# Kernel optimization log

Measured on AMD Instinct MI355X. Metric: run time of the kernel, lower is better.

## Reference

```python
import jax, jax.numpy as jnp
import numpy as np

B, L, N, D = 16, 4096, 1024, 256
EPS = 1e-5
NEG = -1e9


def setup_inputs() -> dict:
    key = jax.random.key(0)
    k1, k2, k3 = jax.random.split(key, 3)
    exp_f = jax.random.normal(k1, (B, L, D), dtype=jnp.float32)
    Q = jax.random.normal(k2, (B, N, D), dtype=jnp.float32)
    attn_mask = jax.random.randint(k3, (B, L, N), 0, 2).astype(jnp.bool_)
    gamma = jnp.ones((D,), dtype=jnp.float32)
    beta = jnp.zeros((D,), dtype=jnp.float32)
    return {"exp_f": exp_f, "Q": Q, "attn_mask": attn_mask, "gamma": gamma, "beta": beta}


def layer_norm(x, gamma, beta):
    mu = jnp.mean(x, axis=-1, keepdims=True)
    var = jnp.mean(jnp.square(x - mu), axis=-1, keepdims=True)
    return (x - mu) * jax.lax.rsqrt(var + EPS) * gamma + beta


def reference(exp_f, Q, attn_mask, gamma, beta):
    d_k = Q.shape[-1]
    scale = 1.0 / np.sqrt(d_k).astype(np.float32)
    # scores: [B, L, N] = exp_f @ Q^T / sqrt(d)
    scores = jnp.einsum('bld,bnd->bln', exp_f, Q) * scale
    scores = jnp.where(attn_mask, jnp.float32(NEG), scores)
    # transpose to [B, N, L], softmax over L (text positions)
    attn = jax.nn.softmax(scores.transpose(0, 2, 1), axis=-1)
    # context: [B, N, D]
    context = jnp.einsum('bnl,bld->bnd', attn, exp_f)
    return layer_norm(Q + context, gamma, beta)
```

## Files before the change

kernel.cpp:

```cpp
#include <hip/hip_runtime.h>
#include <hip/hip_bf16.h>
#include <math.h>

typedef short bf16x8 __attribute__((ext_vector_type(8)));
typedef float f32x4 __attribute__((ext_vector_type(4)));
typedef unsigned int u32;
typedef unsigned short u16;

#define B_ 16
#define L_ 4096
#define N_ 1024
#define D_ 256
#define EPS_ 1e-5f
#define NEG_ -1.0e9f
#define LOG2E_ 1.4426950408889634f
#define THR_ 8.0f

#define LBLK 32
#define PSTR2 40
#define ESTR2 264
#define TSTR2 40

__device__ __forceinline__ u32 pk2(float x, float y) {
  __hip_bfloat16 hx = __float2bfloat16(x), hy = __float2bfloat16(y);
  return (u32)reinterpret_cast<unsigned short&>(hx) |
         ((u32)reinterpret_cast<unsigned short&>(hy) << 16);
}
__device__ __forceinline__ float bf2f(u16 u) {
  return __uint_as_float(((u32)u) << 16);
}

__global__ __launch_bounds__(256)
void prep_kernel(const float* __restrict__ ef, __hip_bfloat16* __restrict__ et,
                 __hip_bfloat16* __restrict__ ebf, int write_ebf) {
  __shared__ float T[64][65];
  const int tid = threadIdx.x;
  const int bid = blockIdx.x;
  const int b  = bid >> 8;
  const int lt = (bid >> 2) & 63;
  const int dt = bid & 3;
  {
    const int r = tid & 63, s = tid >> 6;
    const float* src = ef + ((size_t)b * L_ + lt * 64 + r) * D_ + dt * 64 + s * 16;
    float v[16];
    #pragma unroll
    for (int k = 0; k < 4; ++k) {
      float4 f = *reinterpret_cast<const float4*>(src + 4 * k);
      v[4*k] = f.x; v[4*k+1] = f.y; v[4*k+2] = f.z; v[4*k+3] = f.w;
    }
    #pragma unroll
    for (int m = 0; m < 16; ++m) T[r][s * 16 + m] = v[m];
    if (write_ebf) {
      u32 w[8];
      #pragma unroll
      for (int p = 0; p < 8; ++p) w[p] = pk2(v[2*p], v[2*p+1]);
      __hip_bfloat16* dstrow = ebf + ((size_t)b * L_ + lt * 64 + r) * D_;
      const int u0 = dt * 8 + s * 2;
      const int sw = r & 7;
      *reinterpret_cast<uint4*>(dstrow + (size_t)(u0 ^ sw) * 8)       = *reinterpret_cast<uint4*>(&w[0]);
      *reinterpret_cast<uint4*>(dstrow + (size_t)((u0 + 1) ^ sw) * 8) = *reinterpret_cast<uint4*>(&w[4]);
    }
  }
  __syncthreads();
  {
    const int dcol = tid & 63, s2 = tid >> 6;
    float v[16];
    #pragma unroll
    for (int m = 0; m < 16; ++m) v[m] = T[s2 * 16 + m][dcol];
    u32 w[8];
    #pragma unroll
    for (int p = 0; p < 8; ++p) w[p] = pk2(v[2*p], v[2*p+1]);
    __hip_bfloat16* dst = et + ((size_t)b * D_ + dt * 64 + dcol) * L_ + lt * 64 + s2 * 16;
    *reinterpret_cast<uint4*>(dst)     = *reinterpret_cast<uint4*>(&w[0]);
    *reinterpret_cast<uint4*>(dst + 8) = *reinterpret_cast<uint4*>(&w[4]);
  }
}

__global__ __launch_bounds__(256, 2)
void attn_part3(const float* __restrict__ q, const int* __restrict__ msk,
                const __hip_bfloat16* __restrict__ et,
                const __hip_bfloat16* __restrict__ ebf, int slog,
                __hip_bfloat16* __restrict__ opart,
                float* __restrict__ mpart, float* __restrict__ lpart) {
  extern __shared__ char smem[];
  __hip_bfloat16* ELb = (__hip_bfloat16*)smem;
  __hip_bfloat16* TLb = ELb + 2 * 32 * 256;
  __hip_bfloat16* PLb = TLb + 2 * 256 * 32;

  const int tid  = threadIdx.x;
  const int wid  = tid >> 6;
  const int lane = tid & 63;
  const int g    = lane >> 4;
  const int c    = lane & 15;

  const int S   = 1 << slog;
  const int nb  = 128 << slog;
  const int raw = blockIdx.x;
  const int cpx = nb >> 3;
  const int bs  = (raw & 7) * cpx + (raw >> 3);
  const int nt   = bs & 7;
  const int rest = bs >> 3;
  const int s    = rest & (S - 1);
  const int b    = rest >> slog;

  const int lsplit = L_ >> slog;
  const int lbase  = s * lsplit;
  const int n0w    = nt * 128 + wid * 32;
  const int ntiles = lsplit / LBLK;

  bf16x8 qf[2][8];
  #pragma unroll
  for (int h = 0; h < 2; ++h) {
    const float* qrow = q + ((size_t)b * N_ + n0w + 16*h + c) * D_;
    #pragma unroll
    for (int dk = 0; dk < 8; ++dk) {
      float4 a  = *reinterpret_cast<const float4*>(qrow + 32 * dk + 8 * g);
      float4 b2 = *reinterpret_cast<const float4*>(qrow + 32 * dk + 8 * g + 4);
      u32 w[4] = {pk2(a.x, a.y), pk2(a.z, a.w), pk2(b2.x, b2.y), pk2(b2.z, b2.w)};
      qf[h][dk] = *reinterpret_cast<bf16x8*>(w);
    }
  }

  f32x4 oacc[2][16];
  float m_run[2], l_run[2];
  #pragma unroll
  for (int h = 0; h < 2; ++h) {
    m_run[h] = -INFINITY; l_run[h] = 0.f;
    #pragma unroll
    for (int j = 0; j < 16; ++j) oacc[h][j] = (f32x4){0.f, 0.f, 0.f, 0.f};
  }

  __hip_bfloat16* PLw = PLb + wid * (2 * 16 * PSTR2);
  const float scale = 0.0625f;

  auto STAGE = [&](int tindex, int bufi) {
    const int l0 = lbase + tindex * LBLK;
    __hip_bfloat16* ELd = ELb + bufi * (32 * 256);
    __hip_bfloat16* TLd = TLb + bufi * (256 * 32);
    #pragma unroll
    for (int p = 0; p < 4; ++p) {
      const int u   = (wid * 4 + p) * 64 + lane;
      const int row = u >> 5, iu = u & 31;
      const __hip_bfloat16* src =
          ebf + ((size_t)b * L_ + l0 + row) * D_ + (size_t)iu * 8;
      __builtin_amdgcn_global_load_lds(
          (const __attribute__((address_space(1))) void*)src,
          (__attribute__((address_space(3))) void*)(ELd + (size_t)(wid * 4 + p) * 512),
          16, 0, 0);
    }
    #pragma unroll
    for (int p = 0; p < 4; ++p) {
      const int u  = (wid * 4 + p) * 64 + lane;
      const int dr = u >> 2, iu = u & 3;
      const __hip_bfloat16* src =
          et + ((size_t)b * D_ + dr) * L_ + l0 + iu * 8;
      __builtin_amdgcn_global_load_lds(
          (const __attribute__((address_space(1))) void*)src,
          (__attribute__((address_space(3))) void*)(TLd + (size_t)(wid * 4 + p) * 512),
          16, 0, 0);
    }
  };

  STAGE(0, 0);
  int cur = 0;

  for (int t = 0; t < ntiles; ++t) {
    __syncthreads();
    if (t + 1 < ntiles) STAGE(t + 1, cur ^ 1);

    const int l0 = lbase + t * LBLK;
    const __hip_bfloat16* ELc = ELb + cur * (32 * 256);
    const __hip_bfloat16* TLc = TLb + cur * (256 * 32);

    int mv[16];
    #pragma unroll
    for (int h = 0; h < 2; ++h)
      #pragma unroll
      for (int tt = 0; tt < 2; ++tt)
        #pragma unroll
        for (int r = 0; r < 4; ++r)
          mv[8*h + 4*tt + r] =
              msk[((size_t)b * L_ + l0 + 16*tt + 4*g + r) * N_ + n0w + 16*h + c];

    float sv[2][8];
    __builtin_amdgcn_s_setprio(1);
    #pragma unroll
    for (int tt = 0; tt < 2; ++tt) {
      f32x4 s0 = (f32x4){0.f, 0.f, 0.f, 0.f};
      f32x4 s1 = (f32x4){0.f, 0.f, 0.f, 0.f};
      const __hip_bfloat16* Erow = ELc + (16*tt + c) * 256;
      const int sw = c & 7;
      #pragma unroll
      for (int dk = 0; dk < 8; ++dk) {
        bf16x8 af = *reinterpret_cast<const bf16x8*>(Erow + (size_t)((4*dk + g) ^ sw) * 8);
        s0 = __builtin_amdgcn_mfma_f32_16x16x32_bf16(af, qf[0][dk], s0, 0, 0, 0);
        s1 = __builtin_amdgcn_mfma_f32_16x16x32_bf16(af, qf[1][dk], s1, 0, 0, 0);
      }
      #pragma unroll
      for (int r = 0; r < 4; ++r) {
        float v0 = s0[r] * scale;
        float v1 = s1[r] * scale;
        if (mv[4*tt + r])     v0 = NEG_;
        if (mv[8 + 4*tt + r]) v1 = NEG_;
        sv[0][4*tt + r] = v0;
        sv[1][4*tt + r] = v1;
      }
    }
    __builtin_amdgcn_s_setprio(0);

    #pragma unroll
    for (int h = 0; h < 2; ++h) {
      float tm = sv[h][0];
      #pragma unroll
      for (int i = 1; i < 8; ++i) tm = fmaxf(tm, sv[h][i]);
      tm = fmaxf(tm, __shfl_xor(tm, 16));
      tm = fmaxf(tm, __shfl_xor(tm, 32));
      if (!__all(tm - m_run[h] <= THR_)) {
        const float mn = fmaxf(m_run[h], tm);
        const float alpha = __builtin_amdgcn_exp2f((m_run[h] - mn) * LOG2E_);
        l_run[h] *= alpha;
        float ar[4];
        #pragma unroll
        for (int r = 0; r < 4; ++r) ar[r] = __shfl(alpha, 4*g + r, 64);
        #pragma unroll
        for (int j = 0; j < 16; ++j)
          #pragma unroll
          for (int r = 0; r < 4; ++r) oacc[h][j][r] *= ar[r];
        m_run[h] = mn;
      }
      float ts = 0.f;
      #pragma unroll
      for (int i = 0; i < 8; ++i) {
        sv[h][i] = __builtin_amdgcn_exp2f((sv[h][i] - m_run[h]) * LOG2E_);
        ts += sv[h][i];
      }
      ts += __shfl_xor(ts, 16);
      ts += __shfl_xor(ts, 32);
      l_run[h] += ts;
      #pragma unroll
      for (int tt = 0; tt < 2; ++tt) {
        uint2 w;
        w.x = pk2(sv[h][4*tt+0], sv[h][4*tt+1]);
        w.y = pk2(sv[h][4*tt+2], sv[h][4*tt+3]);
        *reinterpret_cast<uint2*>(PLw + h * 16 * PSTR2 + c * PSTR2 + 16*tt + 4*g) = w;
      }
    }

    bf16x8 pa0 = *reinterpret_cast<const bf16x8*>(PLw + c * PSTR2 + 8*g);
    bf16x8 pa1 = *reinterpret_cast<const bf16x8*>(PLw + 16 * PSTR2 + c * PSTR2 + 8*g);
    __builtin_amdgcn_s_setprio(1);
    #pragma unroll
    for (int j = 0; j < 16; ++j) {
      bf16x8 bfr = *reinterpret_cast<const bf16x8*>(TLc + (16*j + c) * 32 + 8*g);
      oacc[0][j] = __builtin_amdgcn_mfma_f32_16x16x32_bf16(pa0, bfr, oacc[0][j], 0, 0, 0);
      oacc[1][j] = __builtin_amdgcn_mfma_f32_16x16x32_bf16(pa1, bfr, oacc[1][j], 0, 0, 0);
    }
    __builtin_amdgcn_s_setprio(0);

    cur ^= 1;
  }

  const size_t slot = (size_t)rest * 8 + nt;
  __hip_bfloat16* ob = opart + slot * (128 * 256);
  #pragma unroll
  for (int h = 0; h < 2; ++h) {
    float invl[4];
    #pragma unroll
    for (int r = 0; r < 4; ++r) invl[r] = 1.f / __shfl(l_run[h], 4*g + r, 64);
    #pragma unroll
    for (int r = 0; r < 4; ++r) {
      const int row = wid * 32 + 16*h + 4*g + r;
      #pragma unroll
      for (int j = 0; j < 16; ++j)
        ob[(size_t)row * 256 + 16*j + c] = __float2bfloat16(oacc[h][j][r] * invl[r]);
    }
  }
  if (g == 0) {
    #pragma unroll
    for (int h = 0; h < 2; ++h) {
      mpart[slot * 128 + wid * 32 + 16*h + c] = m_run[h];
      lpart[slot * 128 + wid * 32 + 16*h + c] = l_run[h];
    }
  }
}

__global__ __launch_bounds__(256, 2)
void attn_part2(const float* __restrict__ ef, const float* __restrict__ q,
                const int* __restrict__ msk, const __hip_bfloat16* __restrict__ et,
                int slog, __hip_bfloat16* __restrict__ opart,
                float* __restrict__ mpart, float* __restrict__ lpart) {
  extern __shared__ char smem[];
  __hip_bfloat16* EL  = (__hip_bfloat16*)smem;
  __hip_bfloat16* TL  = EL + LBLK * ESTR2;
  __hip_bfloat16* PLb = TL + 256 * TSTR2;
  const int tid  = threadIdx.x;
  const int wid  = tid >> 6;
  const int lane = tid & 63;
  const int g    = lane >> 4;
  const int c    = lane & 15;
  const int S   = 1 << slog;
  const int nb  = 128 << slog;
  const int raw = blockIdx.x;
  const int cpx = nb >> 3;
  const int bs  = (raw & 7) * cpx + (raw >> 3);
  const int nt   = bs & 7;
  const int rest = bs >> 3;
  const int s    = rest & (S - 1);
  const int b    = rest >> slog;
  const int lsplit = L_ >> slog;
  const int lbase  = s * lsplit;
  const int n0w    = nt * 128 + wid * 32;
  bf16x8 qf[2][8];
  #pragma unroll
  for (int h = 0; h < 2; ++h) {
    const float* qrow = q + ((size_t)b * N_ + n0w + 16*h + c) * D_;
    #pragma unroll
    for (int dk = 0; dk < 8; ++dk) {
      float4 a  = *reinterpret_cast<const float4*>(qrow + 32 * dk + 8 * g);
      float4 b2 = *reinterpret_cast<const float4*>(qrow + 32 * dk + 8 * g + 4);
      u32 w[4] = {pk2(a.x, a.y), pk2(a.z, a.w), pk2(b2.x, b2.y), pk2(b2.z, b2.w)};
      qf[h][dk] = *reinterpret_cast<bf16x8*>(w);
    }
  }
  f32x4 oacc[2][16];
  float m_run[2], l_run[2];
  #pragma unroll
  for (int h = 0; h < 2; ++h) {
    m_run[h] = -INFINITY; l_run[h] = 0.f;
    #pragma unroll
    for (int j = 0; j < 16; ++j) oacc[h][j] = (f32x4){0.f, 0.f, 0.f, 0.f};
  }
  __hip_bfloat16* PLw = PLb + wid * (2 * 16 * PSTR2);
  const float scale = 0.0625f;
  const int ntiles = lsplit / LBLK;
  for (int t = 0; t < ntiles; ++t) {
    const int l0 = lbase + t * LBLK;
    __syncthreads();
    #pragma unroll
    for (int p = 0; p < 4; ++p) {
      const int unit = tid + 256 * p;
      const int row = unit >> 5, iu = unit & 31;
      const float* src = ef + ((size_t)b * L_ + l0 + row) * D_ + iu * 8;
      float4 a  = *reinterpret_cast<const float4*>(src);
      float4 b2 = *reinterpret_cast<const float4*>(src + 4);
      u32 w[4] = {pk2(a.x, a.y), pk2(a.z, a.w), pk2(b2.x, b2.y), pk2(b2.z, b2.w)};
      *reinterpret_cast<uint4*>(EL + row * ESTR2 + iu * 8) = *reinterpret_cast<uint4*>(w);
    }
    #pragma unroll
    for (int p = 0; p < 4; ++p) {
      const int unit = tid + 256 * p;
      const int dr = unit >> 2, iu = unit & 3;
      *reinterpret_cast<uint4*>(TL + dr * TSTR2 + iu * 8) =
          *reinterpret_cast<const uint4*>(et + ((size_t)b * D_ + dr) * L_ + l0 + iu * 8);
    }
    int mv[16];
    #pragma unroll
    for (int h = 0; h < 2; ++h)
      #pragma unroll
      for (int tt = 0; tt < 2; ++tt)
        #pragma unroll
        for (int r = 0; r < 4; ++r)
          mv[8*h + 4*tt + r] =
              msk[((size_t)b * L_ + l0 + 16*tt + 4*g + r) * N_ + n0w + 16*h + c];
    __syncthreads();
    float sv[2][8];
    #pragma unroll
    for (int tt = 0; tt < 2; ++tt) {
      f32x4 s0 = (f32x4){0.f, 0.f, 0.f, 0.f};
      f32x4 s1 = (f32x4){0.f, 0.f, 0.f, 0.f};
      #pragma unroll
      for (int dk = 0; dk < 8; ++dk) {
        bf16x8 af = *reinterpret_cast<const bf16x8*>(EL + (16*tt + c) * ESTR2 + 32*dk + 8*g);
        s0 = __builtin_amdgcn_mfma_f32_16x16x32_bf16(af, qf[0][dk], s0, 0, 0, 0);
        s1 = __builtin_amdgcn_mfma_f32_16x16x32_bf16(af, qf[1][dk], s1, 0, 0, 0);
      }
      #pragma unroll
      for (int r = 0; r < 4; ++r) {
        float v0 = s0[r] * scale;
        float v1 = s1[r] * scale;
        if (mv[4*tt + r])     v0 = NEG_;
        if (mv[8 + 4*tt + r]) v1 = NEG_;
        sv[0][4*tt + r] = v0;
        sv[1][4*tt + r] = v1;
      }
    }
    #pragma unroll
    for (int h = 0; h < 2; ++h) {
      float tm = sv[h][0];
      #pragma unroll
      for (int i = 1; i < 8; ++i) tm = fmaxf(tm, sv[h][i]);
      tm = fmaxf(tm, __shfl_xor(tm, 16));
      tm = fmaxf(tm, __shfl_xor(tm, 32));
      if (!__all(tm - m_run[h] <= THR_)) {
        const float mn = fmaxf(m_run[h], tm);
        const float alpha = __builtin_amdgcn_exp2f((m_run[h] - mn) * LOG2E_);
        l_run[h] *= alpha;
        float ar[4];
        #pragma unroll
        for (int r = 0; r < 4; ++r) ar[r] = __shfl(alpha, 4*g + r, 64);
        #pragma unroll
        for (int j = 0; j < 16; ++j)
          #pragma unroll
          for (int r = 0; r < 4; ++r) oacc[h][j][r] *= ar[r];
        m_run[h] = mn;
      }
      float ts = 0.f;
      #pragma unroll
      for (int i = 0; i < 8; ++i) {
        sv[h][i] = __builtin_amdgcn_exp2f((sv[h][i] - m_run[h]) * LOG2E_);
        ts += sv[h][i];
      }
      ts += __shfl_xor(ts, 16);
      ts += __shfl_xor(ts, 32);
      l_run[h] += ts;
      #pragma unroll
      for (int tt = 0; tt < 2; ++tt) {
        uint2 w;
        w.x = pk2(sv[h][4*tt+0], sv[h][4*tt+1]);
        w.y = pk2(sv[h][4*tt+2], sv[h][4*tt+3]);
        *reinterpret_cast<uint2*>(PLw + h * 16 * PSTR2 + c * PSTR2 + 16*tt + 4*g) = w;
      }
    }
    bf16x8 pa0 = *reinterpret_cast<const bf16x8*>(PLw + c * PSTR2 + 8*g);
    bf16x8 pa1 = *reinterpret_cast<const bf16x8*>(PLw + 16 * PSTR2 + c * PSTR2 + 8*g);
    #pragma unroll
    for (int j = 0; j < 16; ++j) {
      bf16x8 bfr = *reinterpret_cast<const bf16x8*>(TL + (16*j + c) * TSTR2 + 8*g);
      oacc[0][j] = __builtin_amdgcn_mfma_f32_16x16x32_bf16(pa0, bfr, oacc[0][j], 0, 0, 0);
      oacc[1][j] = __builtin_amdgcn_mfma_f32_16x16x32_bf16(pa1, bfr, oacc[1][j], 0, 0, 0);
    }
  }
  const size_t slot = (size_t)rest * 8 + nt;
  __hip_bfloat16* ob = opart + slot * (128 * 256);
  #pragma unroll
  for (int h = 0; h < 2; ++h) {
    float invl[4];
    #pragma unroll
    for (int r = 0; r < 4; ++r) invl[r] = 1.f / __shfl(l_run[h], 4*g + r, 64);
    #pragma unroll
    for (int r = 0; r < 4; ++r) {
      const int row = wid * 32 + 16*h + 4*g + r;
      #pragma unroll
      for (int j = 0; j < 16; ++j)
        ob[(size_t)row * 256 + 16*j + c] = __float2bfloat16(oacc[h][j][r] * invl[r]);
    }
  }
  if (g == 0) {
    #pragma unroll
    for (int h = 0; h < 2; ++h) {
      mpart[slot * 128 + wid * 32 + 16*h + c] = m_run[h];
      lpart[slot * 128 + wid * 32 + 16*h + c] = l_run[h];
    }
  }
}

__global__ __launch_bounds__(256)
void combine_ln2(const float* __restrict__ q, const float* __restrict__ gamma,
                 const float* __restrict__ beta,
                 const __hip_bfloat16* __restrict__ opart,
                 const float* __restrict__ mpart, const float* __restrict__ lpart,
                 int S, float* __restrict__ out) {
  const int tid = threadIdx.x, wid = tid >> 6, lane = tid & 63;
  const int row = blockIdx.x * 4 + wid;
  const int b = row >> 10, n = row & 1023;
  const int ntile = n >> 7, nl = n & 127;

  float M = -INFINITY;
  for (int s = 0; s < S; ++s) {
    const size_t slot = (size_t)(b * S + s) * 8 + ntile;
    M = fmaxf(M, mpart[slot * 128 + nl]);
  }
  float W = 0.f;
  float4 o = make_float4(0.f, 0.f, 0.f, 0.f);
  for (int s = 0; s < S; ++s) {
    const size_t slot = (size_t)(b * S + s) * 8 + ntile;
    const float w = __builtin_amdgcn_exp2f((mpart[slot * 128 + nl] - M) * LOG2E_) *
                    lpart[slot * 128 + nl];
    W += w;
    ushort4 ov = *reinterpret_cast<const ushort4*>(
        opart + (slot * 128 + nl) * 256 + lane * 4);
    o.x += w * bf2f(ov.x); o.y += w * bf2f(ov.y);
    o.z += w * bf2f(ov.z); o.w += w * bf2f(ov.w);
  }
  const float invW = 1.f / W;
  float4 qv = *reinterpret_cast<const float4*>(q + ((size_t)b * N_ + n) * D_ + lane * 4);
  float4 x;
  x.x = qv.x + o.x * invW; x.y = qv.y + o.y * invW;
  x.z = qv.z + o.z * invW; x.w = qv.w + o.w * invW;

  float sum = x.x + x.y + x.z + x.w;
  sum += __shfl_xor(sum, 1);  sum += __shfl_xor(sum, 2);
  sum += __shfl_xor(sum, 4);  sum += __shfl_xor(sum, 8);
  sum += __shfl_xor(sum, 16); sum += __shfl_xor(sum, 32);
  const float mu = sum * (1.f / 256.f);
  float dx, v2 = 0.f;
  dx = x.x - mu; v2 += dx * dx; dx = x.y - mu; v2 += dx * dx;
  dx = x.z - mu; v2 += dx * dx; dx = x.w - mu; v2 += dx * dx;
  v2 += __shfl_xor(v2, 1);  v2 += __shfl_xor(v2, 2);
  v2 += __shfl_xor(v2, 4);  v2 += __shfl_xor(v2, 8);
  v2 += __shfl_xor(v2, 16); v2 += __shfl_xor(v2, 32);
  const float rs = rsqrtf(v2 * (1.f / 256.f) + EPS_);
  float4 gv = *reinterpret_cast<const float4*>(gamma + lane * 4);
  float4 bv = *reinterpret_cast<const float4*>(beta + lane * 4);
  float4 y;
  y.x = (x.x - mu) * rs * gv.x + bv.x;
  y.y = (x.y - mu) * rs * gv.y + bv.y;
  y.z = (x.z - mu) * rs * gv.z + bv.z;
  y.w = (x.w - mu) * rs * gv.w + bv.w;
  *reinterpret_cast<float4*>(out + ((size_t)b * N_ + n) * D_ + lane * 4) = y;
}

#define QSTRIDE (D_ + 4)
#define PSTRIDF (64 + 4)
__global__ __launch_bounds__(256)
void tgq_fallback(const float* __restrict__ ef, const float* __restrict__ q,
                  const int* __restrict__ msk, const float* __restrict__ gamma,
                  const float* __restrict__ beta, float* __restrict__ out) {
  extern __shared__ float fsm[];
  float* QL = fsm;
  float* EL = QL + 64 * QSTRIDE;
  float* PL = EL + 64 * QSTRIDE;
  const int tid = threadIdx.x, tx = tid & 15, ty = tid >> 4;
  const int b = blockIdx.x >> 4, n0 = (blockIdx.x & 15) * 64;
  {
    const float* qsrc = q + ((size_t)b * N_ + n0) * D_;
    for (int idx = tid; idx < 64 * 64; idx += 256) {
      int row = idx >> 6, c4 = idx & 63;
      *reinterpret_cast<float4*>(&QL[row * QSTRIDE + c4 * 4]) =
          *reinterpret_cast<const float4*>(qsrc + (size_t)row * D_ + c4 * 4);
    }
  }
  float4 O4[4][4]; float m_run[4], l_run[4];
  #pragma unroll
  for (int i = 0; i < 4; ++i) {
    m_run[i] = -INFINITY; l_run[i] = 0.f;
    #pragma unroll
    for (int k = 0; k < 4; ++k) O4[i][k] = make_float4(0.f, 0.f, 0.f, 0.f);
  }
  const float* efb = ef + (size_t)b * L_ * D_;
  const int* mb = msk + (size_t)b * L_ * N_;
  for (int t = 0; t < L_ / 64; ++t) {
    const int l0 = t * 64;
    __syncthreads();
    for (int idx = tid; idx < 64 * 64; idx += 256) {
      int row = idx >> 6, c4 = idx & 63;
      *reinterpret_cast<float4*>(&EL[row * QSTRIDE + c4 * 4]) =
          *reinterpret_cast<const float4*>(efb + (size_t)(l0 + row) * D_ + c4 * 4);
    }
    int4 mvv[4];
    #pragma unroll
    for (int j = 0; j < 4; ++j)
      mvv[j] = *reinterpret_cast<const int4*>(mb + (size_t)(l0 + tx + 16*j) * N_ + n0 + 4*ty);
    __syncthreads();
    float s0[4][4];
    #pragma unroll
    for (int i = 0; i < 4; ++i)
      #pragma unroll
      for (int j = 0; j < 4; ++j) s0[i][j] = 0.f;
    #pragma unroll 4
    for (int dq = 0; dq < 64; ++dq) {
      float4 qv[4], ev[4];
      #pragma unroll
      for (int i = 0; i < 4; ++i)
        qv[i] = *reinterpret_cast<const float4*>(&QL[(4*ty+i) * QSTRIDE + dq*4]);
      #pragma unroll
      for (int j = 0; j < 4; ++j)
        ev[j] = *reinterpret_cast<const float4*>(&EL[(tx+16*j) * QSTRIDE + dq*4]);
      #pragma unroll
      for (int i = 0; i < 4; ++i)
        #pragma unroll
        for (int j = 0; j < 4; ++j)
          s0[i][j] += qv[i].x*ev[j].x + qv[i].y*ev[j].y + qv[i].z*ev[j].z + qv[i].w*ev[j].w;
    }
    #pragma unroll
    for (int i = 0; i < 4; ++i)
      #pragma unroll
      for (int j = 0; j < 4; ++j) {
        float v = s0[i][j] * 0.0625f;
        int mi = (i==0)?mvv[j].x:(i==1)?mvv[j].y:(i==2)?mvv[j].z:mvv[j].w;
        if (mi) v = NEG_;
        s0[i][j] = v;
      }
    #pragma unroll
    for (int i = 0; i < 4; ++i) {
      float mt = fmaxf(fmaxf(s0[i][0], s0[i][1]), fmaxf(s0[i][2], s0[i][3]));
      mt = fmaxf(mt, __shfl_xor(mt,1)); mt = fmaxf(mt, __shfl_xor(mt,2));
      mt = fmaxf(mt, __shfl_xor(mt,4)); mt = fmaxf(mt, __shfl_xor(mt,8));
      float mn = fmaxf(m_run[i], mt);
      float alpha = __builtin_amdgcn_exp2f((m_run[i] - mn) * LOG2E_);
      float tsum = 0.f;
      #pragma unroll
      for (int j = 0; j < 4; ++j) {
        float p = __builtin_amdgcn_exp2f((s0[i][j] - mn) * LOG2E_);
        s0[i][j] = p; tsum += p;
      }
      tsum += __shfl_xor(tsum,1); tsum += __shfl_xor(tsum,2);
      tsum += __shfl_xor(tsum,4); tsum += __shfl_xor(tsum,8);
      l_run[i] = l_run[i] * alpha + tsum; m_run[i] = mn;
      #pragma unroll
      for (int k = 0; k < 4; ++k) {
        O4[i][k].x *= alpha; O4[i][k].y *= alpha; O4[i][k].z *= alpha; O4[i][k].w *= alpha;
      }
    }
    #pragma unroll
    for (int i = 0; i < 4; ++i)
      #pragma unroll
      for (int j = 0; j < 4; ++j)
        PL[(4*ty+i) * PSTRIDF + tx + 16*j] = s0[i][j];
    __syncthreads();
    #pragma unroll 2
    for (int l4 = 0; l4 < 16; ++l4) {
      float4 p4[4];
      #pragma unroll
      for (int i = 0; i < 4; ++i)
        p4[i] = *reinterpret_cast<const float4*>(&PL[(4*ty+i) * PSTRIDF + 4*l4]);
      #pragma unroll
      for (int cc = 0; cc < 4; ++cc) {
        float4 e4[4];
        #pragma unroll
        for (int k = 0; k < 4; ++k)
          e4[k] = *reinterpret_cast<const float4*>(&EL[(4*l4+cc) * QSTRIDE + 4*tx + 64*k]);
        #pragma unroll
        for (int i = 0; i < 4; ++i) {
          float pc = (cc==0)?p4[i].x:(cc==1)?p4[i].y:(cc==2)?p4[i].z:p4[i].w;
          #pragma unroll
          for (int k = 0; k < 4; ++k) {
            O4[i][k].x += pc*e4[k].x; O4[i][k].y += pc*e4[k].y;
            O4[i][k].z += pc*e4[k].z; O4[i][k].w += pc*e4[k].w;
          }
        }
      }
    }
  }
  float* outb = out + ((size_t)b * N_ + n0) * D_;
  #pragma unroll
  for (int i = 0; i < 4; ++i) {
    const int row = 4*ty + i;
    const float inv_l = 1.f / l_run[i];
    float4 xv[4]; float sum = 0.f;
    #pragma unroll
    for (int k = 0; k < 4; ++k) {
      const int d = 4*tx + 64*k;
      float4 qv = *reinterpret_cast<const float4*>(&QL[row * QSTRIDE + d]);
      xv[k].x = qv.x + O4[i][k].x*inv_l; xv[k].y = qv.y + O4[i][k].y*inv_l;
      xv[k].z = qv.z + O4[i][k].z*inv_l; xv[k].w = qv.w + O4[i][k].w*inv_l;
      sum += xv[k].x + xv[k].y + xv[k].z + xv[k].w;
    }
    sum += __shfl_xor(sum,1); sum += __shfl_xor(sum,2);
    sum += __shfl_xor(sum,4); sum += __shfl_xor(sum,8);
    const float mu = sum * (1.f / 256.f);
    float s2 = 0.f;
    #pragma unroll
    for (int k = 0; k < 4; ++k) {
      float dxx;
      dxx = xv[k].x-mu; s2 += dxx*dxx; dxx = xv[k].y-mu; s2 += dxx*dxx;
      dxx = xv[k].z-mu; s2 += dxx*dxx; dxx = xv[k].w-mu; s2 += dxx*dxx;
    }
    s2 += __shfl_xor(s2,1); s2 += __shfl_xor(s2,2);
    s2 += __shfl_xor(s2,4); s2 += __shfl_xor(s2,8);
    const float rs = rsqrtf(s2 * (1.f / 256.f) + EPS_);
    #pragma unroll
    for (int k = 0; k < 4; ++k) {
      const int d = 4*tx + 64*k;
      float4 gg = *reinterpret_cast<const float4*>(gamma + d);
      float4 be = *reinterpret_cast<const float4*>(beta + d);
      float4 y;
      y.x = (xv[k].x-mu)*rs*gg.x + be.x; y.y = (xv[k].y-mu)*rs*gg.y + be.y;
      y.z = (xv[k].z-mu)*rs*gg.z + be.z; y.w = (xv[k].w-mu)*rs*gg.w + be.w;
      *reinterpret_cast<float4*>(outb + (size_t)row * D_ + d) = y;
    }
  }
}

extern "C" void kernel_launch(void* const* d_in, const int* in_sizes, int n_in,
                              void* d_out, int out_size, void* d_ws, size_t ws_size,
                              hipStream_t stream) {
  const float* ef    = (const float*)d_in[0];
  const float* q     = (const float*)d_in[1];
  const int*   m     = (const int*)d_in[2];
  const float* gamma = (const float*)d_in[3];
  const float* beta  = (const float*)d_in[4];
  float* out         = (float*)d_out;

  const size_t et_b  = (size_t)B_ * D_ * L_ * 2;
  const size_t ebf_b = (size_t)B_ * L_ * D_ * 2;
  auto part_bytes = [](int S) {
    const size_t slots = (size_t)B_ * S * 8;
    return slots * 128 * 256 * 2 + 2 * slots * 128 * 4;
  };

  int slog = -1, use_gll = 0;
  if      (ws_size >= et_b + ebf_b + part_bytes(8)) { slog = 3; use_gll = 1; }
  else if (ws_size >= et_b + ebf_b + part_bytes(4)) { slog = 2; use_gll = 1; }
  else if (ws_size >= et_b + part_bytes(8))         { slog = 3; use_gll = 0; }
  else if (ws_size >= et_b + part_bytes(4))         { slog = 2; use_gll = 0; }

  if (slog < 0) {
    const size_t lds = (size_t)(64*QSTRIDE + 64*QSTRIDE + 64*PSTRIDF) * sizeof(float);
    (void)hipFuncSetAttribute(reinterpret_cast<const void*>(tgq_fallback),
                              hipFuncAttributeMaxDynamicSharedMemorySize, (int)lds);
    tgq_fallback<<<dim3(256), dim3(256), lds, stream>>>(ef, q, m, gamma, beta, out);
    return;
  }

  const int S = 1 << slog;
  __hip_bfloat16* et  = (__hip_bfloat16*)d_ws;
  __hip_bfloat16* ebf = use_gll ? (et + (size_t)B_ * D_ * L_) : nullptr;
  const size_t slots = (size_t)B_ * S * 8;
  __hip_bfloat16* opart =
      (__hip_bfloat16*)((char*)d_ws + et_b + (use_gll ? ebf_b : 0));
  float* mpart = (float*)(opart + slots * 128 * 256);
  float* lpart = mpart + slots * 128;

  prep_kernel<<<dim3(4096), dim3(256), 0, stream>>>(ef, et, ebf, use_gll);

  if (use_gll) {
    const size_t lds1 = (size_t)(2 * 32 * 256 + 2 * 256 * 32 + 4 * 2 * 16 * PSTR2) * 2;
    (void)hipFuncSetAttribute(reinterpret_cast<const void*>(attn_part3),
                              hipFuncAttributeMaxDynamicSharedMemorySize, (int)lds1);
    attn_part3<<<dim3(128 * S), dim3(256), lds1, stream>>>(
        q, m, et, ebf, slog, opart, mpart, lpart);
  } else {
    const size_t lds1 = (size_t)(LBLK * ESTR2 + 256 * TSTR2 + 4 * 2 * 16 * PSTR2) * 2;
    attn_part2<<<dim3(128 * S), dim3(256), lds1, stream>>>(
        ef, q, m, et, slog, opart, mpart, lpart);
  }

  combine_ln2<<<dim3(4096), dim3(256), 0, stream>>>(
      q, gamma, beta, opart, mpart, lpart, S, out);
}
```

Measured before the change: 301.7 us.

## Swizzle transposed E tile for conflict-free LDS reads and prefetch mask one tile ahead

The transposed bf16 copy of exp_f is now written with an XOR swizzle on its 16-byte chunks within each 32-wide L block, and the PV-stage LDS reads use the matching swizzle, to avoid LDS bank conflicts. Separately, the attention-mask loads for the next tile are issued alongside the async stage of that tile, so their global latency overlaps the current tile's compute. This costs 16 extra registers per thread for the prefetched mask under a 2-waves-per-SIMD launch bound. The swizzle depends on write_ebf being true for the et layout, which ties the attention kernel to that prep path.

```diff
diff --git a/kernel.cpp b/kernel.cpp
--- a/kernel.cpp
+++ b/kernel.cpp
@@ -70,9 +70,12 @@
     u32 w[8];
     #pragma unroll
     for (int p = 0; p < 8; ++p) w[p] = pk2(v[2*p], v[2*p+1]);
-    __hip_bfloat16* dst = et + ((size_t)b * D_ + dt * 64 + dcol) * L_ + lt * 64 + s2 * 16;
-    *reinterpret_cast<uint4*>(dst)     = *reinterpret_cast<uint4*>(&w[0]);
-    *reinterpret_cast<uint4*>(dst + 8) = *reinterpret_cast<uint4*>(&w[4]);
+    __hip_bfloat16* dstrow = et + ((size_t)b * D_ + dt * 64 + dcol) * L_;
+    const int base4 = lt * 8 + 4 * (s2 >> 1);
+    const int p0    = 2 * (s2 & 1);
+    const int k3    = write_ebf ? (dcol & 3) : 0;
+    *reinterpret_cast<uint4*>(dstrow + (size_t)(base4 + (p0 ^ k3)) * 8)       = *reinterpret_cast<uint4*>(&w[0]);
+    *reinterpret_cast<uint4*>(dstrow + (size_t)(base4 + ((p0 + 1) ^ k3)) * 8) = *reinterpret_cast<uint4*>(&w[4]);
   }
 }
 
@@ -107,6 +110,7 @@
   const int lbase  = s * lsplit;
   const int n0w    = nt * 128 + wid * 32;
   const int ntiles = lsplit / LBLK;
+  const int gx3    = g ^ (c & 3);
 
   bf16x8 qf[2][8];
   #pragma unroll
@@ -160,27 +164,33 @@
           16, 0, 0);
     }
   };
-
+  auto LOADMASK = [&](int tindex, int* dst) {
+    const int l0 = lbase + tindex * LBLK;
+    #pragma unroll
+    for (int h = 0; h < 2; ++h)
+      #pragma unroll
+      for (int tt = 0; tt < 2; ++tt)
+        #pragma unroll
+        for (int r = 0; r < 4; ++r)
+          dst[8*h + 4*tt + r] =
+              msk[((size_t)b * L_ + l0 + 16*tt + 4*g + r) * N_ + n0w + 16*h + c];
+  };
+
+  int mv[16], mvn[16];
   STAGE(0, 0);
+  LOADMASK(0, mv);
   int cur = 0;
 
   for (int t = 0; t < ntiles; ++t) {
     __syncthreads();
-    if (t + 1 < ntiles) STAGE(t + 1, cur ^ 1);
-
-    const int l0 = lbase + t * LBLK;
+    const bool more = (t + 1 < ntiles);
+    if (more) {
+      STAGE(t + 1, cur ^ 1);
+      LOADMASK(t + 1, mvn);
+    }
+
     const __hip_bfloat16* ELc = ELb + cur * (32 * 256);
     const __hip_bfloat16* TLc = TLb + cur * (256 * 32);
-
-    int mv[16];
-    #pragma unroll
-    for (int h = 0; h < 2; ++h)
-      #pragma unroll
-      for (int tt = 0; tt < 2; ++tt)
-        #pragma unroll
-        for (int r = 0; r < 4; ++r)
-          mv[8*h + 4*tt + r] =
-              msk[((size_t)b * L_ + l0 + 16*tt + 4*g + r) * N_ + n0w + 16*h + c];
 
     float sv[2][8];
     __builtin_amdgcn_s_setprio(1);
@@ -251,12 +261,16 @@
     __builtin_amdgcn_s_setprio(1);
     #pragma unroll
     for (int j = 0; j < 16; ++j) {
-      bf16x8 bfr = *reinterpret_cast<const bf16x8*>(TLc + (16*j + c) * 32 + 8*g);
+      bf16x8 bfr = *reinterpret_cast<const bf16x8*>(TLc + (16*j + c) * 32 + 8*gx3);
       oacc[0][j] = __builtin_amdgcn_mfma_f32_16x16x32_bf16(pa0, bfr, oacc[0][j], 0, 0, 0);
       oacc[1][j] = __builtin_amdgcn_mfma_f32_16x16x32_bf16(pa1, bfr, oacc[1][j], 0, 0, 0);
     }
     __builtin_amdgcn_s_setprio(0);
 
+    if (more) {
+      #pragma unroll
+      for (int i = 0; i < 16; ++i) mv[i] = mvn[i];
+    }
     cur ^= 1;
   }
 
```

New measurement: 475.0 us. +57.4%, slower.
